# Kernel optimization log

Measured on AMD Instinct MI355X. Metric: run time of the kernel, lower is better.

The kernel has to match this reference:

```python
import jax, jax.numpy as jnp
import numpy as np


def setup_inputs() -> dict:
    key = jax.random.key(0)
    k1, k2, k3, k4 = jax.random.split(key, 4)
    B, OPT, IN, OUT = 16384, 64, 128, 128
    stddev = 1.0 / np.sqrt(IN)
    inputs = jax.random.normal(k1, (B, IN), dtype=jnp.float32)
    # haiku TruncatedNormal(stddev) init approximated with truncated normal
    w = jax.random.truncated_normal(k2, -2.0, 2.0, (OPT, IN, OUT), dtype=jnp.float32) * stddev
    b = jnp.zeros((OPT, OUT), dtype=jnp.float32)  # init=zeros; use random for a nontrivial check
    b = jax.random.normal(k3, (OPT, OUT), dtype=jnp.float32) * 0.02
    indices = jax.random.randint(k4, (B,), 0, OPT, dtype=jnp.int64)
    return {"inputs": inputs, "w": w, "b": b, "indices": indices}


def reference(inputs, w, b, indices):
    # out[i] = inputs[i] @ w[indices[i]] + b[indices[i]]
    # Faithful to vmap(jnp.dot)(inputs, w[indices]): gather per-example weight
    # matrices then batched matvec.
    wg = w[indices]                              # [B, IN, OUT] gathered weights
    out = jnp.einsum('bi,bio->bo', inputs, wg)   # [B, OUT]
    return out + b[indices]
```

## Files before the change

kernel.cpp:

```cpp
#include <hip/hip_runtime.h>


#define B_TOT    16384
#define NOPT     64
#define DIN      128
#define DOUT     128
#define NSLICE   8
#define SLICE_LEN (B_TOT / NSLICE)
#define NTHREADS 256

typedef __attribute__((ext_vector_type(8))) short  short8;
typedef __attribute__((ext_vector_type(4))) float  floatx4;

static __device__ __forceinline__ short f2bf(float f) {
    union { float f; unsigned u; } v; v.f = f;
    unsigned r = v.u + 0x7fffu + ((v.u >> 16) & 1u);
    return (short)(r >> 16);
}

__global__ __launch_bounds__(NTHREADS)
void multilinear_kernel(const float* __restrict__ x,
                        const float* __restrict__ w,
                        const float* __restrict__ bias,
                        const int*   __restrict__ idx,
                        float* __restrict__ out) {
    __shared__ int s_list[SLICE_LEN];
    __shared__ int s_cnt;

    const int bid = blockIdx.x;
    const int o   = bid >> 3;
    const int s   = bid & (NSLICE - 1);
    const int t   = threadIdx.x;

    if (t == 0) s_cnt = 0;
    __syncthreads();

    const int base = s * SLICE_LEN;
    #pragma unroll
    for (int k = 0; k < SLICE_LEN / NTHREADS; ++k) {
        int i = base + t + k * NTHREADS;
        if (idx[i] == o) {
            int p = atomicAdd(&s_cnt, 1);
            s_list[p] = i;
        }
    }
    __syncthreads();
    const int count = s_cnt;
    if (count == 0) return;

    const int wave = t >> 6;
    const int lane = t & 63;
    const int l15  = lane & 15;
    const int quad = lane >> 4;

    const float* wo = w + (size_t)o * DIN * DOUT;
    short8 bfrag[4][2];
    #pragma unroll
    for (int kb = 0; kb < 4; ++kb) {
        #pragma unroll
        for (int nt = 0; nt < 2; ++nt) {
            const int n  = (wave * 2 + nt) * 16 + l15;
            const int k0 = kb * 32 + quad * 8;
            short8 f;
            #pragma unroll
            for (int j = 0; j < 8; ++j)
                f[j] = f2bf(wo[(size_t)(k0 + j) * DOUT + n]);
            bfrag[kb][nt] = f;
        }
    }

    float bv[2];
    #pragma unroll
    for (int nt = 0; nt < 2; ++nt)
        bv[nt] = bias[o * DOUT + (wave * 2 + nt) * 16 + l15];

    const int mtiles = (count + 15) >> 4;
    for (int mt = 0; mt < mtiles; ++mt) {
        int am = mt * 16 + l15;
        int arid = s_list[am < count ? am : count - 1];
        const float* xr = x + (size_t)arid * DIN;

        floatx4 acc[2] = {{0.f,0.f,0.f,0.f},{0.f,0.f,0.f,0.f}};
        #pragma unroll
        for (int kb = 0; kb < 4; ++kb) {
            const int k0 = kb * 32 + quad * 8;
            float4 xa = *(const float4*)(xr + k0);
            float4 xb = *(const float4*)(xr + k0 + 4);
            short8 af;
            af[0] = f2bf(xa.x); af[1] = f2bf(xa.y);
            af[2] = f2bf(xa.z); af[3] = f2bf(xa.w);
            af[4] = f2bf(xb.x); af[5] = f2bf(xb.y);
            af[6] = f2bf(xb.z); af[7] = f2bf(xb.w);
            acc[0] = __builtin_amdgcn_mfma_f32_16x16x32_bf16(af, bfrag[kb][0], acc[0], 0, 0, 0);
            acc[1] = __builtin_amdgcn_mfma_f32_16x16x32_bf16(af, bfrag[kb][1], acc[1], 0, 0, 0);
        }

        #pragma unroll
        for (int r = 0; r < 4; ++r) {
            const int m = mt * 16 + quad * 4 + r;
            if (m < count) {
                const int rid = s_list[m];
                #pragma unroll
                for (int nt = 0; nt < 2; ++nt) {
                    const int n = (wave * 2 + nt) * 16 + l15;
                    out[(size_t)rid * DOUT + n] = acc[nt][r] + bv[nt];
                }
            }
        }
    }
}

extern "C" void kernel_launch(void* const* d_in, const int* in_sizes, int n_in,
                              void* d_out, int out_size, void* d_ws, size_t ws_size,
                              hipStream_t stream) {
    const float* x    = (const float*)d_in[0];
    const float* w    = (const float*)d_in[1];
    const float* bias = (const float*)d_in[2];
    const int*   idx  = (const int*)d_in[3];
    float* out        = (float*)d_out;

    multilinear_kernel<<<NOPT * NSLICE, NTHREADS, 0, stream>>>(x, w, bias, idx, out);
}
```

Baseline: 80.35 us.

## Pre-convert weights to transposed bf16 and stage them in LDS

```diff
diff --git a/kernel.cpp b/kernel.cpp
--- a/kernel.cpp
+++ b/kernel.cpp
@@ -1,13 +1,14 @@
 #include <hip/hip_runtime.h>
 
 
-#define B_TOT    16384
-#define NOPT     64
-#define DIN      128
-#define DOUT     128
-#define NSLICE   8
+#define B_TOT     16384
+#define NOPT      64
+#define DIN       128
+#define DOUT      128
+#define NSLICE    16
 #define SLICE_LEN (B_TOT / NSLICE)
-#define NTHREADS 256
+#define NTHREADS  256
+#define SP        136
 
 typedef __attribute__((ext_vector_type(8))) short  short8;
 typedef __attribute__((ext_vector_type(4))) float  floatx4;
@@ -19,17 +20,37 @@
 }
 
 __global__ __launch_bounds__(NTHREADS)
+void convert_wT_kernel(const float* __restrict__ w, unsigned short* __restrict__ wT) {
+    const int o = blockIdx.x & 63;
+    const int p = blockIdx.x >> 6;
+    const int t = threadIdx.x;
+    const int nn = p * 32 + (t & 31);
+    const float* wo = w + (size_t)o * DIN * DOUT;
+    unsigned short* wto = wT + (size_t)o * DIN * DOUT;
+    #pragma unroll
+    for (int it = 0; it < 2; ++it) {
+        const int c = (t >> 5) + 8 * it;
+        short8 v;
+        #pragma unroll
+        for (int j = 0; j < 8; ++j)
+            v[j] = f2bf(wo[(size_t)(c * 8 + j) * DOUT + nn]);
+        *(short8*)(wto + (size_t)nn * DIN + c * 8) = v;
+    }
+}
+
+__global__ __launch_bounds__(NTHREADS)
 void multilinear_kernel(const float* __restrict__ x,
-                        const float* __restrict__ w,
+                        const unsigned short* __restrict__ wT,
                         const float* __restrict__ bias,
                         const int*   __restrict__ idx,
                         float* __restrict__ out) {
     __shared__ int s_list[SLICE_LEN];
     __shared__ int s_cnt;
+    __shared__ unsigned short s_w[DOUT * SP];
 
     const int bid = blockIdx.x;
-    const int o   = bid >> 3;
-    const int s   = bid & (NSLICE - 1);
+    const int o   = bid & 63;
+    const int s   = bid >> 6;
     const int t   = threadIdx.x;
 
     if (t == 0) s_cnt = 0;
@@ -44,7 +65,18 @@
             s_list[p] = i;
         }
     }
+
+    const unsigned short* wto = wT + (size_t)o * DIN * DOUT;
+    #pragma unroll
+    for (int it = 0; it < 8; ++it) {
+        const int e16 = it * NTHREADS + t;
+        const int n   = e16 >> 4;
+        const int c   = e16 & 15;
+        short8 v = *(const short8*)(wto + (size_t)n * DIN + c * 8);
+        *(short8*)(&s_w[n * SP + c * 8]) = v;
+    }
     __syncthreads();
+
     const int count = s_cnt;
     if (count == 0) return;
 
@@ -53,26 +85,10 @@
     const int l15  = lane & 15;
     const int quad = lane >> 4;
 
-    const float* wo = w + (size_t)o * DIN * DOUT;
-    short8 bfrag[4][2];
-    #pragma unroll
-    for (int kb = 0; kb < 4; ++kb) {
-        #pragma unroll
-        for (int nt = 0; nt < 2; ++nt) {
-            const int n  = (wave * 2 + nt) * 16 + l15;
-            const int k0 = kb * 32 + quad * 8;
-            short8 f;
-            #pragma unroll
-            for (int j = 0; j < 8; ++j)
-                f[j] = f2bf(wo[(size_t)(k0 + j) * DOUT + n]);
-            bfrag[kb][nt] = f;
-        }
-    }
-
-    float bv[2];
-    #pragma unroll
-    for (int nt = 0; nt < 2; ++nt)
-        bv[nt] = bias[o * DOUT + (wave * 2 + nt) * 16 + l15];
+    const int n0 = (wave * 2 + 0) * 16 + l15;
+    const int n1 = (wave * 2 + 1) * 16 + l15;
+    const float bv0 = bias[o * DOUT + n0];
+    const float bv1 = bias[o * DOUT + n1];
 
     const int mtiles = (count + 15) >> 4;
     for (int mt = 0; mt < mtiles; ++mt) {
@@ -80,7 +96,8 @@
         int arid = s_list[am < count ? am : count - 1];
         const float* xr = x + (size_t)arid * DIN;
 
-        floatx4 acc[2] = {{0.f,0.f,0.f,0.f},{0.f,0.f,0.f,0.f}};
+        floatx4 acc0 = {0.f, 0.f, 0.f, 0.f};
+        floatx4 acc1 = {0.f, 0.f, 0.f, 0.f};
         #pragma unroll
         for (int kb = 0; kb < 4; ++kb) {
             const int k0 = kb * 32 + quad * 8;
@@ -91,8 +108,10 @@
             af[2] = f2bf(xa.z); af[3] = f2bf(xa.w);
             af[4] = f2bf(xb.x); af[5] = f2bf(xb.y);
             af[6] = f2bf(xb.z); af[7] = f2bf(xb.w);
-            acc[0] = __builtin_amdgcn_mfma_f32_16x16x32_bf16(af, bfrag[kb][0], acc[0], 0, 0, 0);
-            acc[1] = __builtin_amdgcn_mfma_f32_16x16x32_bf16(af, bfrag[kb][1], acc[1], 0, 0, 0);
+            short8 b0 = *(const short8*)(&s_w[n0 * SP + k0]);
+            short8 b1 = *(const short8*)(&s_w[n1 * SP + k0]);
+            acc0 = __builtin_amdgcn_mfma_f32_16x16x32_bf16(af, b0, acc0, 0, 0, 0);
+            acc1 = __builtin_amdgcn_mfma_f32_16x16x32_bf16(af, b1, acc1, 0, 0, 0);
         }
 
         #pragma unroll
@@ -100,11 +119,8 @@
             const int m = mt * 16 + quad * 4 + r;
             if (m < count) {
                 const int rid = s_list[m];
-                #pragma unroll
-                for (int nt = 0; nt < 2; ++nt) {
-                    const int n = (wave * 2 + nt) * 16 + l15;
-                    out[(size_t)rid * DOUT + n] = acc[nt][r] + bv[nt];
-                }
+                out[(size_t)rid * DOUT + n0] = acc0[r] + bv0;
+                out[(size_t)rid * DOUT + n1] = acc1[r] + bv1;
             }
         }
     }
@@ -118,6 +134,8 @@
     const float* bias = (const float*)d_in[2];
     const int*   idx  = (const int*)d_in[3];
     float* out        = (float*)d_out;
+    unsigned short* wT = (unsigned short*)d_ws;
 
-    multilinear_kernel<<<NOPT * NSLICE, NTHREADS, 0, stream>>>(x, w, bias, idx, out);
+    convert_wT_kernel<<<NOPT * 4, NTHREADS, 0, stream>>>(w, wT);
+    multilinear_kernel<<<NOPT * NSLICE, NTHREADS, 0, stream>>>(x, wT, bias, idx, out);
 }
```

Result: faster. 76.43 us (-4.9%).
